# Kernel optimization log

Hardware: AMD Instinct MI355X
Metric: run time of the kernel (lower is better)

Reference implementation:

```python
import jax, jax.numpy as jnp
import numpy as np

EPS = 1e-05

def exp_map_at_origin(v, c):
    sqrt_c = jnp.sqrt(c)
    v_norm = jnp.maximum(jnp.linalg.norm(v, axis=-1, keepdims=True), EPS)
    return (1.0 / sqrt_c) * jnp.tanh(sqrt_c * v_norm) * (v / v_norm)

def log_map_at_origin(y, c):
    sqrt_c = jnp.sqrt(c)
    y_norm = jnp.maximum(jnp.linalg.norm(y, axis=-1, keepdims=True), EPS)
    y_norm_clamped = jnp.minimum(y_norm, 1.0 / sqrt_c - EPS)
    return (1.0 / sqrt_c) * jnp.arctanh(sqrt_c * y_norm_clamped) * (y / y_norm)

def poincare_distance(x, y, c):
    # x, y: [B, H, S, d]; returns [B, H, S, S]
    sqrt_c = jnp.sqrt(c)
    xns = jnp.sum(x * x, axis=-1, keepdims=True)          # [B,H,S,1]
    yns = jnp.sum(y * y, axis=-1, keepdims=True)          # [B,H,S,1]
    xy = jnp.einsum('bhsd,bhtd->bhst', x, y)
    xnsb = xns                                            # broadcast over t
    ynsb = jnp.swapaxes(yns, -2, -1)                      # [B,H,1,S]
    diff_norm_sq = xnsb - 2.0 * xy + ynsb
    denom = jnp.maximum((1.0 - c * xnsb) * (1.0 - c * ynsb), EPS)
    arg = jnp.maximum(1.0 + 2.0 * c * diff_norm_sq / denom, 1.0 + EPS)
    return (1.0 / sqrt_c) * jnp.arccosh(arg)

def setup_inputs() -> dict:
    key = jax.random.key(0)
    ks = jax.random.split(key, 5)
    B, S, D = 2, 1024, 1024
    x = jax.random.normal(ks[0], (B, S, D), dtype=jnp.float32)
    scale = 0.02
    W_q = scale * jax.random.normal(ks[1], (D, D), dtype=jnp.float32)
    W_k = scale * jax.random.normal(ks[2], (D, D), dtype=jnp.float32)
    W_v = scale * jax.random.normal(ks[3], (D, D), dtype=jnp.float32)
    W_o = scale * jax.random.normal(ks[4], (D, D), dtype=jnp.float32)
    return {
        'x': x, 'W_q': W_q, 'W_k': W_k, 'W_v': W_v, 'W_o': W_o,
        'log_c': jnp.zeros((), jnp.float32),
        'beta': jnp.zeros((), jnp.float32),
        'attention_bias': jnp.zeros((), jnp.float32),
    }

def reference(x, W_q, W_k, W_v, W_o, log_c, beta, attention_bias):
    B, S, D = x.shape
    H = 16
    dh = D // H
    c = jax.nn.softplus(log_c)
    beta_pos = jax.nn.softplus(beta)

    def split_heads(t):  # [B,S,D] -> [B,H,S,dh]
        return jnp.transpose(t.reshape(B, S, H, dh), (0, 2, 1, 3))

    q_t = split_heads(x @ W_q.T)
    k_t = split_heads(x @ W_k.T)
    v_t = split_heads(x @ W_v.T)

    q_h = exp_map_at_origin(q_t, c)
    k_h = exp_map_at_origin(k_t, c)
    v_h = exp_map_at_origin(v_t, c)

    dist = poincare_distance(q_h, k_h, c)                 # [B,H,S,S]
    scores = -beta_pos * dist - attention_bias
    weights = jax.nn.softmax(scores, axis=-1)

    v_tan = log_map_at_origin(v_h, c)
    out_tan = jnp.einsum('bhst,bhtd->bhsd', weights, v_tan)
    out_hyp = exp_map_at_origin(out_tan, c)
    out_heads_tan = log_map_at_origin(out_hyp, c)

    concat = jnp.transpose(out_heads_tan, (0, 2, 1, 3)).reshape(B, S, D)
    return concat @ W_o.T
```

## Files before the change

kernel.cpp:

```cpp
#include <hip/hip_runtime.h>
#include <math.h>


#define EPS_ 1e-5f

constexpr int Ss = 1024, Dd = 1024, Hh = 16, DHh = 64;

typedef __attribute__((ext_vector_type(8))) short bf16x8;
typedef __attribute__((ext_vector_type(4))) short s16x4;
typedef __attribute__((ext_vector_type(4))) float f32x4;

__device__ __forceinline__ float softplusf_(float x) {
    return (x > 20.f) ? x : log1pf(expf(x));
}
__device__ __forceinline__ float waveSum64(float v) {
#pragma unroll
    for (int m = 32; m >= 1; m >>= 1) v += __shfl_xor(v, m, 64);
    return v;
}
__device__ __forceinline__ short f2bf(float f) {
    union { float f; unsigned u; } v; v.f = f;
    unsigned r = v.u + 0x7FFFu + ((v.u >> 16) & 1u);
    return (short)(r >> 16);
}
__device__ __forceinline__ float bf2f(unsigned short h) {
    union { unsigned u; float f; } v; v.u = ((unsigned)h) << 16;
    return v.f;
}
__device__ __forceinline__ unsigned pks(short a, short b) {
    return (unsigned)(unsigned short)a | ((unsigned)(unsigned short)b << 16);
}

#if __has_builtin(__builtin_amdgcn_cvt_pk_bf16_f32)
typedef __attribute__((ext_vector_type(2))) __bf16 bfp2;
__device__ __forceinline__ unsigned cvtpk(float a, float b) {
    union { bfp2 v; unsigned u; } x;
    x.v = __builtin_amdgcn_cvt_pk_bf16_f32(a, b);
    return x.u;
}
#else
__device__ __forceinline__ unsigned cvtpk(float a, float b) { return pks(f2bf(a), f2bf(b)); }
#endif

#if __has_builtin(__builtin_amdgcn_sqrtf)
#define FSQRT __builtin_amdgcn_sqrtf
#else
#define FSQRT sqrtf
#endif
#if __has_builtin(__builtin_amdgcn_logf)
#define FLOG2 __builtin_amdgcn_logf
#else
#define FLOG2 __log2f
#endif
#if __has_builtin(__builtin_amdgcn_exp2f)
#define FEXP2 __builtin_amdgcn_exp2f
#else
#define FEXP2 exp2f
#endif

__device__ __forceinline__ void gload_lds16(const short* gp, short* lp) {
    __builtin_amdgcn_global_load_lds(
        (__attribute__((address_space(1))) void*)(void*)(const_cast<short*>(gp)),
        (__attribute__((address_space(3))) void*)(void*)(lp), 16, 0, 0);
}

__global__ __launch_bounds__(256) void split_all(
    const float* __restrict__ x,  const float* __restrict__ Wq,
    const float* __restrict__ Wk, const float* __restrict__ Wv,
    const float* __restrict__ Wo,
    short* __restrict__ xh,  short* __restrict__ wqh,
    short* __restrict__ wkh, short* __restrict__ wvh, short* __restrict__ woh)
{
    int g = blockIdx.x * 256 + threadIdx.x;
    const float* src; short* dst; int base;
    if (g < 524288)       { src = x;  dst = xh;  base = g; }
    else if (g < 786432)  { src = Wq; dst = wqh; base = g - 524288; }
    else if (g < 1048576) { src = Wk; dst = wkh; base = g - 786432; }
    else if (g < 1310720) { src = Wv; dst = wvh; base = g - 1048576; }
    else                  { src = Wo; dst = woh; base = g - 1310720; }
    float4 v = *(const float4*)(src + (size_t)base * 4);
    uint2 hp; hp.x = cvtpk(v.x, v.y); hp.y = cvtpk(v.z, v.w);
    *(uint2*)(dst + (size_t)base * 4) = hp;
}

__global__ __launch_bounds__(256, 3) void gemm_qkv(
    const short* __restrict__ Ap,
    const short* __restrict__ Wq, const short* __restrict__ Wk, const short* __restrict__ Wv,
    short* __restrict__ qh, short* __restrict__ kh, short* __restrict__ vtT,
    float* __restrict__ qnsT, float2* __restrict__ knpk,
    const float* __restrict__ p_logc)
{
    const int z = blockIdx.z;
    const short* Bp = (z == 0) ? Wq : (z == 1 ? Wk : Wv);
    const int K = 1024;

    __shared__ short As[128 * 64];
    __shared__ short Bs[64 * 64];

    const int tid = threadIdx.x;
    const int wv = tid >> 6, lane = tid & 63, quad = lane >> 4, l15 = lane & 15;
    const int bm = blockIdx.y * 128, bn = blockIdx.x * 64;

    const int lr8 = lane >> 3, lc8 = lane & 7;
    const int swz8 = (lc8 ^ lr8) * 8;

    const short* gAl = Ap + (size_t)(bm + lr8) * K + swz8;
    const short* gBl = Bp + (size_t)(bn + lr8) * K + swz8;

    f32x4 acc[2][4];
#pragma unroll
    for (int mt = 0; mt < 2; mt++)
#pragma unroll
        for (int j = 0; j < 4; j++) acc[mt][j] = (f32x4){0.f, 0.f, 0.f, 0.f};

    for (int k0 = 0; k0 < K; k0 += 64) {
        __syncthreads();
#pragma unroll
        for (int i = 0; i < 4; i++)
            gload_lds16(gAl + (size_t)((wv * 4 + i) * 8) * K + k0, &As[(wv * 4 + i) * 512]);
#pragma unroll
        for (int j = 0; j < 2; j++)
            gload_lds16(gBl + (size_t)((wv * 2 + j) * 8) * K + k0, &Bs[(wv * 2 + j) * 512]);
        __syncthreads();
#pragma unroll
        for (int w = 0; w < 2; w++) {
            const int xs = ((w * 4 + quad) ^ (l15 & 7)) * 8;
            bf16x8 fa0 = *(const bf16x8*)&As[(wv * 32 + l15) * 64 + xs];
            bf16x8 fa1 = *(const bf16x8*)&As[(wv * 32 + 16 + l15) * 64 + xs];
#pragma unroll
            for (int nt = 0; nt < 4; nt++) {
                bf16x8 fb = *(const bf16x8*)&Bs[(nt * 16 + l15) * 64 + xs];
                acc[0][nt] = __builtin_amdgcn_mfma_f32_16x16x32_bf16(fa0, fb, acc[0][nt], 0, 0, 0);
                acc[1][nt] = __builtin_amdgcn_mfma_f32_16x16x32_bf16(fa1, fb, acc[1][nt], 0, 0, 0);
            }
        }
    }

    const float c = softplusf_(p_logc[0]);
    const float sc = sqrtf(c);
    const float twoC = 2.f * c;
    const int h0 = blockIdx.x;

    if (z < 2) {
        short* yout = (z == 0) ? qh : kh;
#pragma unroll
        for (int mt = 0; mt < 2; mt++) {
            const int mbase = bm + wv * 32 + mt * 16;
            float fr[4];
#pragma unroll
            for (int r = 0; r < 4; r++) {
                float s2 = 0.f;
#pragma unroll
                for (int nt = 0; nt < 4; nt++) s2 += acc[mt][nt][r] * acc[mt][nt][r];
#pragma unroll
                for (int mk = 1; mk < 16; mk <<= 1) s2 += __shfl_xor(s2, mk, 64);
                float n = fmaxf(sqrtf(s2), EPS_);
                float fac = tanhf(sc * n) / (sc * n);
                fr[r] = fac;
                if (l15 == 0) {
                    int m = mbase + quad * 4 + r;
                    int bI = m >> 10, s = m & 1023;
                    float yns = s2 * fac * fac;
                    if (z == 0) {
                        qnsT[(size_t)(bI * Hh + h0) * Ss + s] = yns;
                    } else {
                        knpk[(size_t)(bI * Hh + h0) * Ss + s]
                            = make_float2(yns, twoC / (1.f - c * yns));
                    }
                }
            }
#pragma unroll
            for (int nt = 0; nt < 4; nt++)
#pragma unroll
                for (int r = 0; r < 4; r++) {
                    int m = mbase + quad * 4 + r;
                    yout[(size_t)m * Dd + bn + nt * 16 + l15] = f2bf(acc[mt][nt][r] * fr[r]);
                }
        }
    } else {
#pragma unroll
        for (int mt = 0; mt < 2; mt++) {
            const int mbase = bm + wv * 32 + mt * 16;
            float tr[4];
#pragma unroll
            for (int r = 0; r < 4; r++) {
                float s2 = 0.f;
#pragma unroll
                for (int nt = 0; nt < 4; nt++) s2 += acc[mt][nt][r] * acc[mt][nt][r];
#pragma unroll
                for (int mk = 1; mk < 16; mk <<= 1) s2 += __shfl_xor(s2, mk, 64);
                float n = fmaxf(sqrtf(s2), EPS_);
                float fac = tanhf(sc * n) / (sc * n);
                float yn = n * fac;
                float ycl = fminf(yn, 1.f / sc - EPS_);
                float f2 = atanhf(sc * ycl) / (sc * fmaxf(yn, EPS_));
                tr[r] = fac * f2;
            }
            const int m0 = mbase + quad * 4;
            const int bI = m0 >> 10, s0 = m0 & 1023;
#pragma unroll
            for (int nt = 0; nt < 4; nt++) {
                int d = nt * 16 + l15;
                uint2 pk;
                pk.x = cvtpk(acc[mt][nt][0] * tr[0], acc[mt][nt][1] * tr[1]);
                pk.y = cvtpk(acc[mt][nt][2] * tr[2], acc[mt][nt][3] * tr[3]);
                *(uint2*)&vtT[((size_t)(bI * Hh + h0) * DHh + d) * Ss + s0] = pk;
            }
        }
    }
}

__global__ __launch_bounds__(256) void attn_mfma(
    const short* __restrict__ qh, const short* __restrict__ kh, const short* __restrict__ vtT,
    const float* __restrict__ qnsT, const float2* __restrict__ knpk,
    unsigned short* __restrict__ Opart, float* __restrict__ lpart,
    const float* __restrict__ p_logc, const float* __restrict__ p_beta)
{
    const float c = softplusf_(p_logc[0]);
    const float sc = sqrtf(c);
    const float bp = softplusf_(p_beta[0]);
    const float nkc = -bp / sc;
    const float cap = 2.f * c * 1e5f;
    const float onePlus = 1.f + EPS_;

    const int h = blockIdx.y, b = blockIdx.z;
    const int kr = blockIdx.x & 3, qt = blockIdx.x >> 2;
    const int tid = threadIdx.x;
    const int wv = tid >> 6, lane = tid & 63;
    const int quad = lane >> 4, l15 = lane & 15;
    const int bh = b * Hh + h;
    const int q = qt * 64 + wv * 16 + l15;

    __shared__ short Ks[2][64][72];
    __shared__ short Vt[2][64][72];

    const short* qb = qh + (size_t)(b * Ss + q) * Dd + h * DHh + quad * 8;
    bf16x8 qf0 = *(const bf16x8*)qb;
    bf16x8 qf1 = *(const bf16x8*)(qb + 32);

    const float qn = qnsT[(size_t)bh * Ss + q];
    const float irq = 1.f / (1.f - c * qn);

    f32x4 O4[4];
#pragma unroll
    for (int nt = 0; nt < 4; nt++) O4[nt] = (f32x4){0.f, 0.f, 0.f, 0.f};
    float lac = 0.f;

    const int tbase = kr * 256;
    const int sr = tid >> 2, sseg = (tid & 3) * 16;
    const int vhi = sseg & 32;
    const int vup = (sseg & 16) ? 4 : 0;
    const short* kgp = kh + (size_t)(b * Ss + tbase + sr) * Dd + h * DHh + sseg;
    const short* vgp = vtT + ((size_t)bh * DHh + sr) * Ss + tbase + sseg;
    const float2* nb = knpk + (size_t)bh * Ss;

    bf16x8 kA0 = *(const bf16x8*)kgp;
    bf16x8 kA1 = *(const bf16x8*)(kgp + 8);
    bf16x8 vA0 = *(const bf16x8*)vgp;
    bf16x8 vA1 = *(const bf16x8*)(vgp + 8);
    {
        *(bf16x8*)&Ks[0][sr][sseg]     = kA0;
        *(bf16x8*)&Ks[0][sr][sseg + 8] = kA1;
        short* vrow = &Vt[0][sr][0];
        *(s16x4*)(vrow + vhi + vup)      = __builtin_shufflevector(vA0, vA0, 0, 1, 2, 3);
        *(s16x4*)(vrow + vhi + 8 + vup)  = __builtin_shufflevector(vA0, vA0, 4, 5, 6, 7);
        *(s16x4*)(vrow + vhi + 16 + vup) = __builtin_shufflevector(vA1, vA1, 0, 1, 2, 3);
        *(s16x4*)(vrow + vhi + 24 + vup) = __builtin_shufflevector(vA1, vA1, 4, 5, 6, 7);
    }
    __syncthreads();

    for (int ch = 0; ch < 4; ch++) {
        const int cur = ch & 1, nxt = cur ^ 1;
        const int t0 = tbase + ch * 64;

        if (ch < 3) {
            kA0 = *(const bf16x8*)(kgp + (size_t)((ch + 1) * 64) * Dd);
            kA1 = *(const bf16x8*)(kgp + (size_t)((ch + 1) * 64) * Dd + 8);
            vA0 = *(const bf16x8*)(vgp + (ch + 1) * 64);
            vA1 = *(const bf16x8*)(vgp + (ch + 1) * 64 + 8);
        }

        f32x4 n0[4], n1[4];
#pragma unroll
        for (int nt = 0; nt < 4; nt++) {
            const float2* np = nb + t0 + nt * 16 + quad * 4;
            n0[nt] = *(const f32x4*)np;
            n1[nt] = *(const f32x4*)(np + 2);
        }

        f32x4 acc[4];
#pragma unroll
        for (int nt = 0; nt < 4; nt++) {
            bf16x8 k0 = *(const bf16x8*)&Ks[cur][nt * 16 + l15][quad * 8];
            bf16x8 k1 = *(const bf16x8*)&Ks[cur][nt * 16 + l15][32 + quad * 8];
            f32x4 a = (f32x4){0.f, 0.f, 0.f, 0.f};
            a = __builtin_amdgcn_mfma_f32_16x16x32_bf16(k0, qf0, a, 0, 0, 0);
            a = __builtin_amdgcn_mfma_f32_16x16x32_bf16(k1, qf1, a, 0, 0, 0);
            acc[nt] = a;
        }

        float sv[4][4];
#pragma unroll
        for (int nt = 0; nt < 4; nt++) {
#pragma unroll
            for (int r = 0; r < 4; r++) {
                float kn   = (r < 2) ? n0[nt][(r & 1) * 2]     : n1[nt][(r & 1) * 2];
                float ik2c = (r < 2) ? n0[nt][(r & 1) * 2 + 1] : n1[nt][(r & 1) * 2 + 1];
                float dns = (qn + kn) - 2.f * acc[nt][r];
                float co  = fminf(irq * ik2c, cap);
                float arg = fmaxf(fmaf(co, dns, 1.f), onePlus);
                float u   = arg + FSQRT(fmaf(arg, arg, -1.f));
                float p   = FEXP2(nkc * FLOG2(u));
                sv[nt][r] = p;
                lac += p;
            }
        }

        union { unsigned u[4]; bf16x8 v; } p0, p1;
        p0.u[0] = cvtpk(sv[0][0], sv[0][1]); p0.u[1] = cvtpk(sv[0][2], sv[0][3]);
        p0.u[2] = cvtpk(sv[1][0], sv[1][1]); p0.u[3] = cvtpk(sv[1][2], sv[1][3]);
        p1.u[0] = cvtpk(sv[2][0], sv[2][1]); p1.u[1] = cvtpk(sv[2][2], sv[2][3]);
        p1.u[2] = cvtpk(sv[3][0], sv[3][1]); p1.u[3] = cvtpk(sv[3][2], sv[3][3]);

#pragma unroll
        for (int nt = 0; nt < 4; nt++) {
            bf16x8 v0 = *(const bf16x8*)&Vt[cur][nt * 16 + l15][quad * 8];
            bf16x8 v1 = *(const bf16x8*)&Vt[cur][nt * 16 + l15][32 + quad * 8];
            O4[nt] = __builtin_amdgcn_mfma_f32_16x16x32_bf16(v0, p0.v, O4[nt], 0, 0, 0);
            O4[nt] = __builtin_amdgcn_mfma_f32_16x16x32_bf16(v1, p1.v, O4[nt], 0, 0, 0);
        }

        if (ch < 3) {
            *(bf16x8*)&Ks[nxt][sr][sseg]     = kA0;
            *(bf16x8*)&Ks[nxt][sr][sseg + 8] = kA1;
            short* vrow = &Vt[nxt][sr][0];
            *(s16x4*)(vrow + vhi + vup)      = __builtin_shufflevector(vA0, vA0, 0, 1, 2, 3);
            *(s16x4*)(vrow + vhi + 8 + vup)  = __builtin_shufflevector(vA0, vA0, 4, 5, 6, 7);
            *(s16x4*)(vrow + vhi + 16 + vup) = __builtin_shufflevector(vA1, vA1, 0, 1, 2, 3);
            *(s16x4*)(vrow + vhi + 24 + vup) = __builtin_shufflevector(vA1, vA1, 4, 5, 6, 7);
            __syncthreads();
        }
    }

    lac += __shfl_xor(lac, 16, 64);
    lac += __shfl_xor(lac, 32, 64);
    unsigned short* ob = Opart + (((size_t)bh * 4 + kr) * Ss + q) * DHh;
#pragma unroll
    for (int nt = 0; nt < 4; nt++) {
        uint2 pk;
        pk.x = cvtpk(O4[nt][0], O4[nt][1]);
        pk.y = cvtpk(O4[nt][2], O4[nt][3]);
        *(uint2*)(ob + nt * 16 + quad * 4) = pk;
    }
    if (lane < 16)
        lpart[((size_t)bh * 4 + kr) * Ss + qt * 64 + wv * 16 + lane] = lac;
}

__global__ __launch_bounds__(256) void attn_combine(
    const unsigned short* __restrict__ Opart, const float* __restrict__ lpart,
    short* __restrict__ ccb, const float* __restrict__ p_logc)
{
    const float c = softplusf_(p_logc[0]);
    const float sc = sqrtf(c);
    const int wv = threadIdx.x >> 6, d = threadIdx.x & 63;
    const int task = blockIdx.x * 4 + wv;
    const int bh = task >> 10, s = task & 1023;

    float O = 0.f, l = 0.f;
#pragma unroll
    for (int k = 0; k < 4; k++) {
        O += bf2f(Opart[(((size_t)bh * 4 + k) * Ss + s) * DHh + d]);
        l += lpart[((size_t)bh * 4 + k) * Ss + s];
    }
    float ot = O / l;

    float t2 = waveSum64(ot * ot);
    float n = fmaxf(sqrtf(t2), EPS_);
    float fac = tanhf(sc * n) / (sc * n);
    float y2 = t2 * fac * fac;
    float yn = fmaxf(sqrtf(y2), EPS_);
    float ycl = fminf(yn, 1.f / sc - EPS_);
    float fac2 = atanhf(sc * ycl) / (sc * yn);
    float tot = fac * fac2;

    int b = bh >> 4, hh = bh & 15;
    ccb[(size_t)(b * Ss + s) * Dd + hh * DHh + d] = f2bf(ot * tot);
}

__global__ __launch_bounds__(256, 6) void gemm_out(
    const short* __restrict__ Ap, const short* __restrict__ Bp,
    float* __restrict__ Cp)
{
    const int K = 1024, N = 1024;
    __shared__ short As[64 * 64];
    __shared__ short Bs[64 * 64];
    const int tid = threadIdx.x;
    const int wv = tid >> 6, lane = tid & 63, quad = lane >> 4, l15 = lane & 15;
    const int bm = blockIdx.y * 64, bn = blockIdx.x * 64;

    const int lr8 = lane >> 3, lc8 = lane & 7;
    const int swz8 = (lc8 ^ lr8) * 8;

    const short* gAl = Ap + (size_t)(bm + lr8) * K + swz8;
    const short* gBl = Bp + (size_t)(bn + lr8) * K + swz8;

    f32x4 acc[4];
#pragma unroll
    for (int j = 0; j < 4; j++) acc[j] = (f32x4){0.f, 0.f, 0.f, 0.f};

    for (int k0 = 0; k0 < K; k0 += 64) {
        __syncthreads();
#pragma unroll
        for (int j = 0; j < 2; j++) {
            gload_lds16(gAl + (size_t)((wv * 2 + j) * 8) * K + k0, &As[(wv * 2 + j) * 512]);
            gload_lds16(gBl + (size_t)((wv * 2 + j) * 8) * K + k0, &Bs[(wv * 2 + j) * 512]);
        }
        __syncthreads();
#pragma unroll
        for (int w = 0; w < 2; w++) {
            const int xs = ((w * 4 + quad) ^ (l15 & 7)) * 8;
            bf16x8 fa = *(const bf16x8*)&As[(wv * 16 + l15) * 64 + xs];
#pragma unroll
            for (int nt = 0; nt < 4; nt++) {
                bf16x8 fb = *(const bf16x8*)&Bs[(nt * 16 + l15) * 64 + xs];
                acc[nt] = __builtin_amdgcn_mfma_f32_16x16x32_bf16(fa, fb, acc[nt], 0, 0, 0);
            }
        }
    }
#pragma unroll
    for (int nt = 0; nt < 4; nt++)
#pragma unroll
        for (int r = 0; r < 4; r++)
            Cp[(size_t)(bm + wv * 16 + quad * 4 + r) * N + bn + nt * 16 + l15] = acc[nt][r];
}

extern "C" void kernel_launch(void* const* d_in, const int* in_sizes, int n_in,
                              void* d_out, int out_size, void* d_ws, size_t ws_size,
                              hipStream_t stream)
{
    const float* x    = (const float*)d_in[0];
    const float* Wq   = (const float*)d_in[1];
    const float* Wk   = (const float*)d_in[2];
    const float* Wv   = (const float*)d_in[3];
    const float* Wo   = (const float*)d_in[4];
    const float* logc = (const float*)d_in[5];
    const float* beta = (const float*)d_in[6];
    float* out = (float*)d_out;

    const size_t M2 = 2097152, M1 = 1048576;
    short* ws    = (short*)d_ws;
    short* xh    = ws;
    short* wqh   = xh + M2;
    short* wkh   = wqh + M1;
    short* wvh   = wkh + M1;
    short* woh   = wvh + M1;
    short* qh    = woh + M1;
    short* kh    = qh + M2;
    short* vtT   = kh + M2;
    float* qnsT  = (float*)(vtT + M2);
    float2* knpk = (float2*)(qnsT + 32768);
    float* lpart = (float*)(knpk + 32768);
    unsigned short* Opart = (unsigned short*)(lpart + 131072);
    short* ccb   = xh;

    split_all<<<dim3(6144), 256, 0, stream>>>(x, Wq, Wk, Wv, Wo, xh, wqh, wkh, wvh, woh);
    gemm_qkv<<<dim3(16, 16, 3), 256, 0, stream>>>(xh, wqh, wkh, wvh,
        qh, kh, vtT, qnsT, knpk, logc);
    attn_mfma<<<dim3(64, 16, 2), 256, 0, stream>>>(qh, kh, vtT, qnsT, knpk,
        Opart, lpart, logc, beta);
    attn_combine<<<dim3(8192), 256, 0, stream>>>(Opart, lpart, ccb, logc);
    gemm_out<<<dim3(16, 32), 256, 0, stream>>>(ccb, woh, out);
}
```

Before: 172.1 us.

## Load K/V fragments directly from global, drop LDS staging, halve key split

The attention kernel no longer stages K and V tiles through double-buffered shared memory with barriers. Each wave now loads its MFMA operand fragments straight from global memory. To make those V loads contiguous, the QKV GEMM writes vtT with a permuted sequence order. The key range is split into 2 parts instead of 4, with each block looping over 512 keys, and the combine kernel and workspace offsets are updated to match. This removes LDS traffic and syncs but makes the four waves load K/V redundantly from global/L2, and it halves the grid, so fewer blocks are available to hide latency.

After: 208.5 us. 21.2% more time.

```diff
diff --git a/kernel.cpp b/kernel.cpp
--- a/kernel.cpp
+++ b/kernel.cpp
@@ -198,19 +198,22 @@
             }
             const int m0 = mbase + quad * 4;
             const int bI = m0 >> 10, s0 = m0 & 1023;
+            const int w6 = s0 & 63;
+            const int s0p = (s0 & ~63)
+                          | ((w6 >> 5) * 32 + ((w6 & 15) >> 2) * 8 + ((w6 >> 4) & 1) * 4);
 #pragma unroll
             for (int nt = 0; nt < 4; nt++) {
                 int d = nt * 16 + l15;
                 uint2 pk;
                 pk.x = cvtpk(acc[mt][nt][0] * tr[0], acc[mt][nt][1] * tr[1]);
                 pk.y = cvtpk(acc[mt][nt][2] * tr[2], acc[mt][nt][3] * tr[3]);
-                *(uint2*)&vtT[((size_t)(bI * Hh + h0) * DHh + d) * Ss + s0] = pk;
-            }
-        }
-    }
-}
-
-__global__ __launch_bounds__(256) void attn_mfma(
+                *(uint2*)&vtT[((size_t)(bI * Hh + h0) * DHh + d) * Ss + s0p] = pk;
+            }
+        }
+    }
+}
+
+__global__ __launch_bounds__(256, 3) void attn_mfma(
     const short* __restrict__ qh, const short* __restrict__ kh, const short* __restrict__ vtT,
     const float* __restrict__ qnsT, const float2* __restrict__ knpk,
     unsigned short* __restrict__ Opart, float* __restrict__ lpart,
@@ -224,16 +227,13 @@
     const float onePlus = 1.f + EPS_;
 
     const int h = blockIdx.y, b = blockIdx.z;
-    const int kr = blockIdx.x & 3, qt = blockIdx.x >> 2;
+    const int kr = blockIdx.x & 1, qt = blockIdx.x >> 1;
     const int tid = threadIdx.x;
     const int wv = tid >> 6, lane = tid & 63;
     const int quad = lane >> 4, l15 = lane & 15;
     const int bh = b * Hh + h;
     const int q = qt * 64 + wv * 16 + l15;
 
-    __shared__ short Ks[2][64][72];
-    __shared__ short Vt[2][64][72];
-
     const short* qb = qh + (size_t)(b * Ss + q) * Dd + h * DHh + quad * 8;
     bf16x8 qf0 = *(const bf16x8*)qb;
     bf16x8 qf1 = *(const bf16x8*)(qb + 32);
@@ -246,40 +246,21 @@
     for (int nt = 0; nt < 4; nt++) O4[nt] = (f32x4){0.f, 0.f, 0.f, 0.f};
     float lac = 0.f;
 
-    const int tbase = kr * 256;
-    const int sr = tid >> 2, sseg = (tid & 3) * 16;
-    const int vhi = sseg & 32;
-    const int vup = (sseg & 16) ? 4 : 0;
-    const short* kgp = kh + (size_t)(b * Ss + tbase + sr) * Dd + h * DHh + sseg;
-    const short* vgp = vtT + ((size_t)bh * DHh + sr) * Ss + tbase + sseg;
+    const int tbase = kr * 512;
     const float2* nb = knpk + (size_t)bh * Ss;
-
-    bf16x8 kA0 = *(const bf16x8*)kgp;
-    bf16x8 kA1 = *(const bf16x8*)(kgp + 8);
-    bf16x8 vA0 = *(const bf16x8*)vgp;
-    bf16x8 vA1 = *(const bf16x8*)(vgp + 8);
-    {
-        *(bf16x8*)&Ks[0][sr][sseg]     = kA0;
-        *(bf16x8*)&Ks[0][sr][sseg + 8] = kA1;
-        short* vrow = &Vt[0][sr][0];
-        *(s16x4*)(vrow + vhi + vup)      = __builtin_shufflevector(vA0, vA0, 0, 1, 2, 3);
-        *(s16x4*)(vrow + vhi + 8 + vup)  = __builtin_shufflevector(vA0, vA0, 4, 5, 6, 7);
-        *(s16x4*)(vrow + vhi + 16 + vup) = __builtin_shufflevector(vA1, vA1, 0, 1, 2, 3);
-        *(s16x4*)(vrow + vhi + 24 + vup) = __builtin_shufflevector(vA1, vA1, 4, 5, 6, 7);
-    }
-    __syncthreads();
-
-    for (int ch = 0; ch < 4; ch++) {
-        const int cur = ch & 1, nxt = cur ^ 1;
+    const short* kb = kh + (size_t)(b * Ss + tbase + l15) * Dd + h * DHh + quad * 8;
+    const short* vb = vtT + ((size_t)bh * DHh + l15) * Ss + tbase + quad * 8;
+
+    for (int ch = 0; ch < 8; ch++) {
         const int t0 = tbase + ch * 64;
 
-        if (ch < 3) {
-            kA0 = *(const bf16x8*)(kgp + (size_t)((ch + 1) * 64) * Dd);
-            kA1 = *(const bf16x8*)(kgp + (size_t)((ch + 1) * 64) * Dd + 8);
-            vA0 = *(const bf16x8*)(vgp + (ch + 1) * 64);
-            vA1 = *(const bf16x8*)(vgp + (ch + 1) * 64 + 8);
-        }
-
+        bf16x8 k0[4], k1[4];
+#pragma unroll
+        for (int nt = 0; nt < 4; nt++) {
+            const short* p = kb + (size_t)(ch * 64 + nt * 16) * Dd;
+            k0[nt] = *(const bf16x8*)p;
+            k1[nt] = *(const bf16x8*)(p + 32);
+        }
         f32x4 n0[4], n1[4];
 #pragma unroll
         for (int nt = 0; nt < 4; nt++) {
@@ -291,12 +272,18 @@
         f32x4 acc[4];
 #pragma unroll
         for (int nt = 0; nt < 4; nt++) {
-            bf16x8 k0 = *(const bf16x8*)&Ks[cur][nt * 16 + l15][quad * 8];
-            bf16x8 k1 = *(const bf16x8*)&Ks[cur][nt * 16 + l15][32 + quad * 8];
             f32x4 a = (f32x4){0.f, 0.f, 0.f, 0.f};
-            a = __builtin_amdgcn_mfma_f32_16x16x32_bf16(k0, qf0, a, 0, 0, 0);
-            a = __builtin_amdgcn_mfma_f32_16x16x32_bf16(k1, qf1, a, 0, 0, 0);
+            a = __builtin_amdgcn_mfma_f32_16x16x32_bf16(k0[nt], qf0, a, 0, 0, 0);
+            a = __builtin_amdgcn_mfma_f32_16x16x32_bf16(k1[nt], qf1, a, 0, 0, 0);
             acc[nt] = a;
+        }
+
+        bf16x8 v0[4], v1[4];
+#pragma unroll
+        for (int nt = 0; nt < 4; nt++) {
+            const short* p = vb + (size_t)(nt * 16) * Ss + ch * 64;
+            v0[nt] = *(const bf16x8*)p;
+            v1[nt] = *(const bf16x8*)(p + 32);
         }
 
         float sv[4][4];
@@ -324,27 +311,14 @@
 
 #pragma unroll
         for (int nt = 0; nt < 4; nt++) {
-            bf16x8 v0 = *(const bf16x8*)&Vt[cur][nt * 16 + l15][quad * 8];
-            bf16x8 v1 = *(const bf16x8*)&Vt[cur][nt * 16 + l15][32 + quad * 8];
-            O4[nt] = __builtin_amdgcn_mfma_f32_16x16x32_bf16(v0, p0.v, O4[nt], 0, 0, 0);
-            O4[nt] = __builtin_amdgcn_mfma_f32_16x16x32_bf16(v1, p1.v, O4[nt], 0, 0, 0);
-        }
-
-        if (ch < 3) {
-            *(bf16x8*)&Ks[nxt][sr][sseg]     = kA0;
-            *(bf16x8*)&Ks[nxt][sr][sseg + 8] = kA1;
-            short* vrow = &Vt[nxt][sr][0];
-            *(s16x4*)(vrow + vhi + vup)      = __builtin_shufflevector(vA0, vA0, 0, 1, 2, 3);
-            *(s16x4*)(vrow + vhi + 8 + vup)  = __builtin_shufflevector(vA0, vA0, 4, 5, 6, 7);
-            *(s16x4*)(vrow + vhi + 16 + vup) = __builtin_shufflevector(vA1, vA1, 0, 1, 2, 3);
-            *(s16x4*)(vrow + vhi + 24 + vup) = __builtin_shufflevector(vA1, vA1, 4, 5, 6, 7);
-            __syncthreads();
+            O4[nt] = __builtin_amdgcn_mfma_f32_16x16x32_bf16(v0[nt], p0.v, O4[nt], 0, 0, 0);
+            O4[nt] = __builtin_amdgcn_mfma_f32_16x16x32_bf16(v1[nt], p1.v, O4[nt], 0, 0, 0);
         }
     }
 
     lac += __shfl_xor(lac, 16, 64);
     lac += __shfl_xor(lac, 32, 64);
-    unsigned short* ob = Opart + (((size_t)bh * 4 + kr) * Ss + q) * DHh;
+    unsigned short* ob = Opart + (((size_t)bh * 2 + kr) * Ss + q) * DHh;
 #pragma unroll
     for (int nt = 0; nt < 4; nt++) {
         uint2 pk;
@@ -353,7 +327,7 @@
         *(uint2*)(ob + nt * 16 + quad * 4) = pk;
     }
     if (lane < 16)
-        lpart[((size_t)bh * 4 + kr) * Ss + qt * 64 + wv * 16 + lane] = lac;
+        lpart[((size_t)bh * 2 + kr) * Ss + qt * 64 + wv * 16 + lane] = lac;
 }
 
 __global__ __launch_bounds__(256) void attn_combine(
@@ -368,9 +342,9 @@
 
     float O = 0.f, l = 0.f;
 #pragma unroll
-    for (int k = 0; k < 4; k++) {
-        O += bf2f(Opart[(((size_t)bh * 4 + k) * Ss + s) * DHh + d]);
-        l += lpart[((size_t)bh * 4 + k) * Ss + s];
+    for (int k = 0; k < 2; k++) {
+        O += bf2f(Opart[(((size_t)bh * 2 + k) * Ss + s) * DHh + d]);
+        l += lpart[((size_t)bh * 2 + k) * Ss + s];
     }
     float ot = O / l;
 
@@ -460,13 +434,13 @@
     float* qnsT  = (float*)(vtT + M2);
     float2* knpk = (float2*)(qnsT + 32768);
     float* lpart = (float*)(knpk + 32768);
-    unsigned short* Opart = (unsigned short*)(lpart + 131072);
+    unsigned short* Opart = (unsigned short*)(lpart + 65536);
     short* ccb   = xh;
 
     split_all<<<dim3(6144), 256, 0, stream>>>(x, Wq, Wk, Wv, Wo, xh, wqh, wkh, wvh, woh);
     gemm_qkv<<<dim3(16, 16, 3), 256, 0, stream>>>(xh, wqh, wkh, wvh,
         qh, kh, vtT, qnsT, knpk, logc);
-    attn_mfma<<<dim3(64, 16, 2), 256, 0, stream>>>(qh, kh, vtT, qnsT, knpk,
+    attn_mfma<<<dim3(32, 16, 2), 256, 0, stream>>>(qh, kh, vtT, qnsT, knpk,
         Opart, lpart, logc, beta);
     attn_combine<<<dim3(8192), 256, 0, stream>>>(Opart, lpart, ccb, logc);
     gemm_out<<<dim3(16, 32), 256, 0, stream>>>(ccb, woh, out);
```
